# Performance work log

Measured on AMD Instinct MI355X. Metric: run time of the kernel, lower is better.

The kernel has to match this reference:

```python
import jax, jax.numpy as jnp
import numpy as np

B, N, C = 8, 2048, 512


def setup_inputs() -> dict:
    key = jax.random.key(0)
    ks = jax.random.split(key, 8)
    s = 1.0 / np.sqrt(C)
    return {
        "x": jax.random.normal(ks[0], (B, N, C), dtype=jnp.float32),
        "Wq": jax.random.normal(ks[1], (C, C), dtype=jnp.float32) * s,
        "Wk": jax.random.normal(ks[2], (C, C), dtype=jnp.float32) * s,
        "Wv": jax.random.normal(ks[3], (C, C), dtype=jnp.float32) * s,
        "W1": jax.random.normal(ks[4], (C, C), dtype=jnp.float32) * s,
        "W2": jax.random.normal(ks[5], (C, C), dtype=jnp.float32) * s,
        "gamma": jax.random.normal(ks[6], (1,), dtype=jnp.float32),
        "beta_p": jax.random.normal(ks[7], (1,), dtype=jnp.float32),
    }


def reference(x, Wq, Wk, Wv, W1, W2, gamma, beta_p):
    # torch.nn.Linear(bias=False): y = x @ W.T  with W of shape [out, in]
    q = jnp.einsum('bnc,dc->bnd', x, Wq)  # [B,N,C]
    k = jnp.einsum('bnc,dc->bnd', x, Wk)
    v = jnp.einsum('bnc,dc->bnd', x, Wv)
    # scores[b,i,j] = q_i . k_j ; softmax over dim=1 (the i axis), as in source
    scores = jnp.einsum('bic,bjc->bij', q, k)        # [B,N,N]
    attn = jax.nn.softmax(scores, axis=1)            # normalize over i
    # bmm(v^T, attn): out[b,c,j] = sum_i v[b,i,c] * attn[b,i,j]; permuted back -> [B,N,C]
    att_out = jnp.einsum('bic,bij->bjc', v, attn)    # [B,N,C]
    o = gamma * att_out + x                          # gamma-scaled residual
    h = jax.nn.relu(jnp.einsum('bnc,dc->bnd', o, W1))
    o = beta_p * jnp.einsum('bnc,dc->bnd', h, W2) + o
    return o
```

## Files before the change

kernel.cpp:

```cpp
#include <hip/hip_runtime.h>
#include <stdint.h>

#define DEVINL __device__ __forceinline__

typedef short short8_t __attribute__((ext_vector_type(8)));
typedef float f32x4_t  __attribute__((ext_vector_type(4)));
typedef _Float16 half8_t __attribute__((ext_vector_type(8)));
typedef unsigned short u16;

static constexpr int  Bn = 8;
static constexpr int  Nn = 2048;
static constexpr int  Cn = 512;
static constexpr int  Mn = Bn * Nn;
static constexpr long NC = (long)Nn * Cn;
static constexpr long NNe = (long)Nn * Nn;
static constexpr long CC = (long)Cn * Cn;
static constexpr long MC = (long)Mn * Cn;

DEVINL u16 f32_to_f16(float f) {
  _Float16 h = (_Float16)f;
  u16 r; __builtin_memcpy(&r, &h, 2);
  return r;
}

DEVINL void mfma_f16(f32x4_t& d, short8_t a, short8_t b) {
  asm("v_mfma_f32_16x16x32_f16 %0, %1, %2, %0" : "+v"(d) : "v"(a), "v"(b));
}

#define GLOAD_LDS16(G, L)                                                      \
  __builtin_amdgcn_global_load_lds(                                            \
      (const __attribute__((address_space(1))) void*)(G),                      \
      (__attribute__((address_space(3))) void*)(L), 16, 0, 0)

__global__ __launch_bounds__(256) void conv_x_kernel(const float* __restrict__ src,
                                                     u16* __restrict__ f16, int n4) {
  int i = blockIdx.x * 256 + threadIdx.x;
  if (i >= n4) return;
  float4 v = ((const float4*)src)[i];
  ((ushort4*)f16)[i] = make_ushort4(f32_to_f16(v.x), f32_to_f16(v.y),
                                    f32_to_f16(v.z), f32_to_f16(v.w));
}

struct W5 { const float* p[5]; };
__global__ __launch_bounds__(256) void conv_w_kernel(W5 ws, u16* __restrict__ f16,
                                                     int n4each) {
  const int w = blockIdx.y;
  const int i = blockIdx.x * 256 + threadIdx.x;
  if (i >= n4each) return;
  float4 v = ((const float4*)ws.p[w])[i];
  ((ushort4*)f16)[(long)w * (CC / 4) + i] =
      make_ushort4(f32_to_f16(v.x), f32_to_f16(v.y), f32_to_f16(v.z), f32_to_f16(v.w));
}

enum { EPI_QKV = 0, EPI_SF16 = 2, EPI_PV = 3, EPI_RELU = 4, EPI_FFN2 = 5 };

template <int BM, int BN, int EPI, int SW>
__global__ __launch_bounds__(256) void gemm_k(
    const u16* Ah, const u16* Bh,
    int K, int outld, void* out0, void* out1,
    const float* aux, const float* scal,
    int batch0, long azStride, long bzStride, long ozStride) {
  constexpr int BK = 32;
  constexpr int ABYTES = BM * BK * 2;
  constexpr int BBYTES = BN * BK * 2;
  constexpr int PB = ABYTES + BBYTES;
  constexpr int FM = BM / 32, FN = BN / 32;
  constexpr int TP = 136;
  constexpr int LDSB = (EPI == EPI_QKV && 2 * PB < BN * TP * 2) ? BN * TP * 2 : 2 * PB;

  __shared__ __align__(1024) char lds[LDSB];

  const int tid = threadIdx.x;
  const int l   = tid & 63;
  const int wid = tid >> 6;

  int bx, byy, bz;
  {
    const int gx = gridDim.x, gy = gridDim.y, gz = gridDim.z;
    const int lid = blockIdx.x + gx * (blockIdx.y + gy * blockIdx.z);
    if (SW == 0) {
      const int c = lid & 7, s = lid >> 3;
      const int nyz = gy * gz;
      const int xi = s / nyz, yz = s - xi * nyz;
      bx = c + 8 * xi; byy = yz % gy; bz = yz / gy;
    } else if (SW == 1) {
      bz = lid & 7;
      const int s = lid >> 3;
      byy = s % gy; bx = s / gy;
    } else {
      const int cpx = gx >> 3;
      bx = (blockIdx.x & 7) * cpx + (blockIdx.x >> 3);
      byy = blockIdx.y; bz = blockIdx.z;
    }
  }

  const int batch = batch0 + bz;
  const int brow  = bx * BM;
  const int bcol  = byy * BN;

  Ah += (long)bz * azStride;
  Bh += (long)bz * bzStride;

  const int wr = (wid >> 1) * (BM / 2);
  const int wc = (wid & 1) * (BN / 2);
  const int rsel = l & 15;
  const int koff = (l >> 4) * 16;

  f32x4_t acc[FM][FN];
  const f32x4_t zero = {0.f, 0.f, 0.f, 0.f};
#pragma unroll
  for (int m = 0; m < FM; ++m)
#pragma unroll
    for (int n = 0; n < FN; ++n) acc[m][n] = zero;

  auto stage = [&](const u16* g, int gld, int row0, int k0, char* dst, int nrows) {
    const int nchunk = nrows / 16;
#pragma unroll
    for (int ci0 = 0; ci0 < nchunk; ci0 += 4) {
      const int ci = ci0 + wid;
      if (ci < nchunk) {
        const u16* src = g + (long)(row0 + ci * 16 + (l >> 2)) * gld + (k0 + (l & 3) * 8);
        GLOAD_LDS16(src, dst + ci * 1024);
      }
    }
  };
  auto stageAll = [&](int k0, char* b) {
    stage(Ah, K, brow, k0, b, BM);
    stage(Bh, K, bcol, k0, b + ABYTES, BN);
  };

  stageAll(0, lds);
  __syncthreads();
  int cur = 0;
  for (int k0 = 0; k0 < K; k0 += BK) {
    char* bb = lds + cur * PB;
    if (k0 + BK < K) stageAll(k0 + BK, lds + (cur ^ 1) * PB);

    short8_t af[FM], bf[FN];
#pragma unroll
    for (int m = 0; m < FM; ++m)
      af[m] = *(const short8_t*)(bb + (wr + m * 16 + rsel) * (BK * 2) + koff);
#pragma unroll
    for (int n = 0; n < FN; ++n)
      bf[n] = *(const short8_t*)(bb + ABYTES + (wc + n * 16 + rsel) * (BK * 2) + koff);
#pragma unroll
    for (int m = 0; m < FM; ++m)
#pragma unroll
      for (int n = 0; n < FN; ++n) mfma_f16(acc[m][n], af[m], bf[n]);
    __syncthreads();
    cur ^= 1;
  }

  const float sc0 = scal ? scal[0] : 0.0f;
  const int crow = (l >> 4) * 4;
  const int ccol = l & 15;

  if (EPI == EPI_QKV && bz == 2) {
    u16* t = (u16*)lds;
#pragma unroll
    for (int m = 0; m < FM; ++m)
#pragma unroll
      for (int n = 0; n < FN; ++n) {
        ushort4 pk = make_ushort4(f32_to_f16(acc[m][n][0]), f32_to_f16(acc[m][n][1]),
                                  f32_to_f16(acc[m][n][2]), f32_to_f16(acc[m][n][3]));
        *(ushort4*)&t[(wc + n * 16 + ccol) * TP + (wr + m * 16 + crow)] = pk;
      }
    __syncthreads();
    const int cl = tid >> 1, hf = tid & 1;
    const long b = brow >> 11;
    u16* dst = (u16*)out1 +
               ((b * Cn + bcol + cl) * (long)Nn + (brow & 2047) + hf * 64);
    const u16* srcT = &t[cl * TP + hf * 64];
#pragma unroll
    for (int i = 0; i < 8; ++i)
      ((uint4*)dst)[i] = *(const uint4*)(srcT + i * 8);
    return;
  }

#pragma unroll
  for (int m = 0; m < FM; ++m)
#pragma unroll
    for (int n = 0; n < FN; ++n)
#pragma unroll
      for (int j = 0; j < 4; ++j) {
        const int r = brow + wr + m * 16 + crow + j;
        const int c = bcol + wc + n * 16 + ccol;
        const float v = acc[m][n][j];
        if (EPI == EPI_QKV) {
          ((u16*)out0)[(long)bz * MC + (long)r * outld + c] = f32_to_f16(v);
        } else if (EPI == EPI_SF16) {
          ((u16*)out0 + (long)bz * ozStride)[(long)r * outld + c] = f32_to_f16(v);
        } else if (EPI == EPI_PV) {
          const long gi = ((long)batch * Nn + r) * Cn + c;
          const float val = sc0 * v + aux[gi];
          ((float*)out0)[gi] = val;
          ((u16*)out1)[gi] = f32_to_f16(val);
        } else if (EPI == EPI_RELU) {
          const float val = v > 0.f ? v : 0.f;
          ((u16*)out0)[(long)r * outld + c] = f32_to_f16(val);
        } else {
          const long gi = (long)r * Cn + c;
          ((float*)out0)[gi] = sc0 * v + aux[gi];
        }
      }
}

__global__ __launch_bounds__(256) void softmax_k(const u16* sc, u16* attn) {
  const long base = (long)blockIdx.y * NNe + (long)blockIdx.x * Nn;
  const int tid = threadIdx.x;
  const int l = tid & 63, wid = tid >> 6;
  half8_t v = ((const half8_t*)(sc + base))[tid];
  float f[8];
#pragma unroll
  for (int i = 0; i < 8; ++i) f[i] = (float)v[i];
  float mx = f[0];
#pragma unroll
  for (int i = 1; i < 8; ++i) mx = fmaxf(mx, f[i]);
#pragma unroll
  for (int o = 32; o > 0; o >>= 1) mx = fmaxf(mx, __shfl_xor(mx, o));
  __shared__ float red[8];
  if (l == 0) red[wid] = mx;
  __syncthreads();
  mx = fmaxf(fmaxf(red[0], red[1]), fmaxf(red[2], red[3]));
  float p[8];
  float s = 0.f;
#pragma unroll
  for (int i = 0; i < 8; ++i) { p[i] = __expf(f[i] - mx); s += p[i]; }
#pragma unroll
  for (int o = 32; o > 0; o >>= 1) s += __shfl_xor(s, o);
  if (l == 0) red[4 + wid] = s;
  __syncthreads();
  s = red[4] + red[5] + red[6] + red[7];
  const float inv = 1.0f / s;
  __align__(16) u16 o8[8];
#pragma unroll
  for (int i = 0; i < 8; ++i) o8[i] = f32_to_f16(p[i] * inv);
  ((uint4*)(attn + base))[tid] = *(const uint4*)o8;
}

extern "C" void kernel_launch(void* const* d_in, const int* in_sizes, int n_in,
                              void* d_out, int out_size, void* d_ws, size_t ws_size,
                              hipStream_t stream) {
  const float* x  = (const float*)d_in[0];
  const float* gamma = (const float*)d_in[6];
  const float* beta  = (const float*)d_in[7];
  float* out = (float*)d_out;

  char* ws = (char*)d_ws;
  size_t off = 0;
  auto alloc = [&](size_t bytes) {
    char* p = ws + off;
    off += (bytes + 1023) & ~(size_t)1023;
    return p;
  };
  u16* x16  = (u16*)alloc((size_t)MC * 2);
  u16* w16A = (u16*)alloc((size_t)5 * CC * 2);
  u16* qk16 = (u16*)alloc((size_t)2 * MC * 2);
  u16* vT   = (u16*)alloc((size_t)MC * 2);
  u16* o16  = (u16*)alloc((size_t)MC * 2);
  u16* h16  = (u16*)alloc((size_t)MC * 2);
  const size_t baseOff = off;

  int zAtt = 8;
  while (zAtt > 1 &&
         baseOff + (size_t)zAtt * (NNe * 2 + 1024 + NNe * 2 + 1024) > ws_size)
    zAtt >>= 1;
  u16* scoresT = (u16*)alloc((size_t)zAtt * NNe * 2);
  u16* attnT   = (u16*)alloc((size_t)zAtt * NNe * 2);
  u16* q16 = qk16;
  u16* k16 = qk16 + (size_t)MC;

  conv_x_kernel<<<dim3(MC / 4 / 256), 256, 0, stream>>>(x, x16, MC / 4);
  W5 w5 = {{(const float*)d_in[1], (const float*)d_in[2], (const float*)d_in[3],
            (const float*)d_in[4], (const float*)d_in[5]}};
  conv_w_kernel<<<dim3(CC / 4 / 256, 5), 256, 0, stream>>>(w5, w16A, CC / 4);

  gemm_k<128,128,EPI_QKV,0><<<dim3(Mn/128, Cn/128, 3), 256, 0, stream>>>(
      x16, w16A, Cn, Cn, qk16, vT, nullptr, nullptr, 0, 0, CC, 0);

  if (zAtt == 8) {
    gemm_k<128,128,EPI_SF16,1><<<dim3(Nn/128, Nn/128, 8), 256, 0, stream>>>(
        k16, q16, Cn, Nn, scoresT, nullptr, nullptr, nullptr, 0, NC, NC, NNe);
    softmax_k<<<dim3(Nn, 8), 256, 0, stream>>>(scoresT, attnT);
    gemm_k<128,128,EPI_PV,1><<<dim3(Nn/128, Cn/128, 8), 256, 0, stream>>>(
        attnT, vT, Nn, Cn, out, o16, x, gamma, 0, NNe, NC, 0);
  } else {
    for (int b0 = 0; b0 < Bn; b0 += zAtt) {
      gemm_k<128,128,EPI_SF16,2><<<dim3(Nn/128, Nn/128, zAtt), 256, 0, stream>>>(
          k16 + (long)b0 * NC, q16 + (long)b0 * NC,
          Cn, Nn, scoresT, nullptr, nullptr, nullptr, b0, NC, NC, NNe);
      softmax_k<<<dim3(Nn, zAtt), 256, 0, stream>>>(scoresT, attnT);
      gemm_k<128,128,EPI_PV,2><<<dim3(Nn/128, Cn/128, zAtt), 256, 0, stream>>>(
          attnT, vT + (long)b0 * NC, Nn, Cn, out, o16, x, gamma,
          b0, NNe, NC, 0);
    }
  }

  gemm_k<128,128,EPI_RELU,0><<<dim3(Mn/128, Cn/128, 1), 256, 0, stream>>>(
      o16, w16A + 3 * CC, Cn, Cn, h16, nullptr, nullptr, nullptr, 0, 0, 0, 0);
  gemm_k<128,128,EPI_FFN2,0><<<dim3(Mn/128, Cn/128, 1), 256, 0, stream>>>(
      h16, w16A + 4 * CC, Cn, Cn, out, nullptr, out, beta, 0, 0, 0, 0);
}
```

Measured before the change: 245.2 us.

## Swizzle LDS tiles and use partial vmcnt waits with split barriers

```diff
diff --git a/kernel.cpp b/kernel.cpp
--- a/kernel.cpp
+++ b/kernel.cpp
@@ -104,7 +104,7 @@
   const int wr = (wid >> 1) * (BM / 2);
   const int wc = (wid & 1) * (BN / 2);
   const int rsel = l & 15;
-  const int koff = (l >> 4) * 16;
+  const int rofs = (((l >> 4) ^ ((rsel >> 1) & 3)) & 3) * 16;
 
   f32x4_t acc[FM][FN];
   const f32x4_t zero = {0.f, 0.f, 0.f, 0.f};
@@ -115,11 +115,12 @@
 
   auto stage = [&](const u16* g, int gld, int row0, int k0, char* dst, int nrows) {
     const int nchunk = nrows / 16;
+    const int cb = ((l & 3) ^ ((l >> 3) & 3)) * 8;
 #pragma unroll
     for (int ci0 = 0; ci0 < nchunk; ci0 += 4) {
       const int ci = ci0 + wid;
       if (ci < nchunk) {
-        const u16* src = g + (long)(row0 + ci * 16 + (l >> 2)) * gld + (k0 + (l & 3) * 8);
+        const u16* src = g + (long)(row0 + ci * 16 + (l >> 2)) * gld + (k0 + cb);
         GLOAD_LDS16(src, dst + ci * 1024);
       }
     }
@@ -130,24 +131,40 @@
   };
 
   stageAll(0, lds);
-  __syncthreads();
   int cur = 0;
   for (int k0 = 0; k0 < K; k0 += BK) {
     char* bb = lds + cur * PB;
-    if (k0 + BK < K) stageAll(k0 + BK, lds + (cur ^ 1) * PB);
+    if (k0 + BK < K) {
+      stageAll(k0 + BK, lds + (cur ^ 1) * PB);
+      __builtin_amdgcn_sched_barrier(0);
+      asm volatile("s_waitcnt vmcnt(4)" ::: "memory");
+    } else {
+      __builtin_amdgcn_sched_barrier(0);
+      asm volatile("s_waitcnt vmcnt(0)" ::: "memory");
+    }
+    __builtin_amdgcn_sched_barrier(0);
+    __builtin_amdgcn_s_barrier();
+    asm volatile("" ::: "memory");
+    __builtin_amdgcn_sched_barrier(0);
 
     short8_t af[FM], bf[FN];
 #pragma unroll
     for (int m = 0; m < FM; ++m)
-      af[m] = *(const short8_t*)(bb + (wr + m * 16 + rsel) * (BK * 2) + koff);
+      af[m] = *(const short8_t*)(bb + (wr + m * 16 + rsel) * (BK * 2) + rofs);
 #pragma unroll
     for (int n = 0; n < FN; ++n)
-      bf[n] = *(const short8_t*)(bb + ABYTES + (wc + n * 16 + rsel) * (BK * 2) + koff);
+      bf[n] = *(const short8_t*)(bb + ABYTES + (wc + n * 16 + rsel) * (BK * 2) + rofs);
+    __builtin_amdgcn_s_setprio(1);
 #pragma unroll
     for (int m = 0; m < FM; ++m)
 #pragma unroll
       for (int n = 0; n < FN; ++n) mfma_f16(acc[m][n], af[m], bf[n]);
-    __syncthreads();
+    __builtin_amdgcn_s_setprio(0);
+
+    __builtin_amdgcn_sched_barrier(0);
+    asm volatile("" ::: "memory");
+    __builtin_amdgcn_s_barrier();
+    __builtin_amdgcn_sched_barrier(0);
     cur ^= 1;
   }
 
```

New measurement: 243.5 us. About the same (-0.7%).
